# Kernel optimization log

Measured on AMD Instinct MI355X. Metric: run time of the kernel, lower is better.

Reference implementation:

```python
import jax, jax.numpy as jnp
import numpy as np

NT, NS, NF, NG, NH, ND, HS = 365, 128, 6, 16, 8, 366, 256
EPS = 1e-6


def _divide_p(p, t1, t2):
    # func.divideP: rain/snow partition via arccos temperature interpolation
    r = jnp.clip((t1 + t2) / jnp.maximum(t2 - t1, EPS), -1.0, 1.0)
    vf = jnp.arccos(r) / jnp.pi
    vf = jnp.where(t1 >= 0, 0.0, vf)
    vf = jnp.where(t2 <= 0, 1.0, vf)
    return p * vf, p * (1.0 - vf)  # Ps (snow), Pl (liquid)


def _hard_sigmoid(x):
    return jnp.clip(x / 6.0 + 0.5, 0.0, 1.0)


def setup_inputs():
    key = jax.random.key(0)
    ks = jax.random.split(key, 11)
    prcp = jax.random.uniform(ks[0], (NT, NS)) * 10.0
    evp = jax.random.uniform(ks[1], (NT, NS)) * 5.0
    t1 = jax.random.normal(ks[2], (NT, NS)) * 10.0
    t2 = t1 + jax.random.uniform(ks[3], (NT, NS)) * 10.0 + 0.1
    rad = jax.random.normal(ks[4], (NT, NS))
    hum = jax.random.normal(ks[5], (NT, NS))
    x = jnp.stack([prcp, evp, t1, t2, rad, hum], axis=-1)  # (NT, NS, 6)
    xc = jax.random.normal(ks[6], (NS, NG))

    def lin(k, fan_out, fan_in):
        b = 1.0 / np.sqrt(fan_in)
        kw, kb = jax.random.split(k)
        return (jax.random.uniform(kw, (fan_out, fan_in), minval=-b, maxval=b),
                jax.random.uniform(kb, (fan_out,), minval=-b, maxval=b))

    W_fc, b_fc = lin(ks[7], HS, NG)
    W_g, b_g = lin(ks[8], NH * 6, HS)
    W_kin, b_kin = lin(ks[9], HS, 4)
    W_kout, b_kout = lin(ks[10], NH * 1, HS)
    return dict(x=x, xc=xc, W_fc=W_fc, b_fc=b_fc, W_g=W_g, b_g=b_g,
                W_kin=W_kin, b_kin=b_kin, W_kout=W_kout, b_kout=b_kout)


def reference(x, xc, W_fc, b_fc, W_g, b_g, W_kin, b_kin, W_kout, b_kout):
    prcp, evp, t1, t2 = x[..., 0], x[..., 1], x[..., 2], x[..., 3]
    ps, pl = _divide_p(prcp, t1, t2)  # (NT, NS)
    f = x[..., 2:]  # (NT, NS, 4) time-varying features T1,T2,Rad,Hum

    # getParam (eval mode -> DropMask is identity)
    state = xc @ W_fc.T + b_fc                                   # (NS, HS)
    pk = jnp.tanh(f @ W_kin.T + b_kin + state) @ W_kout.T + b_kout  # (NT, NS, NH)
    pg = jnp.tanh(state) @ W_g.T + b_g                           # (NS, 6*NH)
    km = jnp.exp(pk)                                             # melt rate
    gk = jnp.exp(pg[:, 0:NH]) / 100.0                            # recession
    gl = jnp.exp(pg[:, NH:2 * NH]) * 100.0                       # capacity
    qb = jax.nn.relu(pg[:, 2 * NH:3 * NH]) / 10.0                # baseflow
    ga = jax.nn.softmax(pg[:, 3 * NH:4 * NH], axis=-1)           # bucket areas
    gi = _hard_sigmoid(pg[:, 4 * NH:5 * NH]) / 2.0               # infiltration frac
    ge = jax.nn.relu(pg[:, 5 * NH:6 * NH])                       # evap factor

    sf0 = jnp.zeros((NS, NH), x.dtype)
    d0 = jnp.zeros((NS, NH, ND), x.dtype)

    @jax.checkpoint
    def step(carry, inp):
        sf, d = carry
        ps_t, pl_t, ev_t, km_t = inp
        # snow bucket
        sf1 = sf + ps_t[:, None]
        melt = jnp.minimum(sf1, km_t)
        sf_new = sf1 - melt
        w_in = melt + pl_t[:, None] * gi           # inflow to soil (NS, NH)
        e_pot = ev_t[:, None] * ge
        # StorAge-Selection: age-rank shift, oldest bin pools
        d_sh = jnp.concatenate([w_in[..., None], d[..., :-1]], axis=-1)
        d_sh = d_sh.at[..., -1].add(d[..., -1])
        s = d_sh.sum(-1)
        # evaporation, uniform over ages, capped by storage
        f_ev = jnp.clip(e_pot / jnp.maximum(s, EPS), 0.0, 1.0)
        d1 = d_sh * (1.0 - f_ev[..., None])
        s1 = s * (1.0 - f_ev)
        # surface spill above capacity gl
        q_s = jax.nn.relu(s1 - gl)
        f_s = q_s / jnp.maximum(s1, EPS)
        d2 = d1 * (1.0 - f_s[..., None])
        s2 = s1 - q_s
        # uniform-SAS subsurface discharge
        q_sub = jnp.minimum(s2 * gk + qb, s2)
        f_q = q_sub / jnp.maximum(s2, EPS)
        q_age = d2 * f_q[..., None]                # flux[1]: per-age outflow
        q_age = q_age.at[..., 0].add(q_s)
        d_new = d2 * (1.0 - f_q[..., None])
        q = jnp.sum(q_age.sum(-1) * ga, axis=-1)   # area-weighted discharge (NS,)
        return (sf_new, d_new), q

    (_, _), q_pred = jax.lax.scan(step, (sf0, d0), (ps, pl, evp, km))
    return q_pred  # (NT, NS)
```

## Files before the change

kernel.cpp:

```cpp
#include <hip/hip_runtime.h>
#include <math.h>

#define NT 365
#define NT2 368
#define NS 128
#define NG 16
#define NH 8
#define HS 256
#define NSNH (NS * NH)
#define EPSC 1e-6f
#define TSTRIDE 96
#define TCH 46

#define WS_PRM 0
#define WS_P   8192

__device__ __forceinline__ float fast_rcp(float v) {
#if __has_builtin(__builtin_amdgcn_rcpf)
    return __builtin_amdgcn_rcpf(v);
#else
    return 1.f / v;
#endif
}
__device__ __forceinline__ float fast_tanh(float xv) {
    float e = __expf(2.f * xv);
    return 1.f - 2.f * fast_rcp(e + 1.f);
}
__device__ __forceinline__ float acos_over_pi(float r) {
    float ax = fabsf(r);
    float p = sqrtf(1.f - ax) *
              (0.49995890f + ax * (-0.06751697f + ax * (0.02363862f + ax * -0.00596153f)));
    return r < 0.f ? 1.f - p : p;
}

__global__ __launch_bounds__(256) void k_main(
    const float* __restrict__ x, const float* __restrict__ xc,
    const float* __restrict__ W_fc, const float* __restrict__ b_fc,
    const float* __restrict__ W_g, const float* __restrict__ b_g,
    const float* __restrict__ W_kin, const float* __restrict__ b_kin,
    const float* __restrict__ W_kout, const float* __restrict__ b_kout,
    float* __restrict__ prm, float* __restrict__ Pf)
{
    __shared__ float us[HS];
    __shared__ float ts[HS];
    __shared__ __align__(16) float4 wkin_lds[HS];
    __shared__ float wko_lds[8 * 260];
    __shared__ __align__(16) float lds_u[4 * 288];
    __shared__ float pgs[6 * NH];

    int tid = threadIdx.x;
    int wave = tid >> 6, lane = tid & 63;
    int s = blockIdx.x & 127;
    int t0 = (blockIdx.x >> 7) * 4 + wave;
    int h = lane >> 3, jg = lane & 7;

    wkin_lds[tid] = ((const float4*)W_kin)[tid];
#pragma unroll
    for (int i = 0; i < 8; ++i) {
        int idx = tid + 256 * i;
        wko_lds[(idx >> 8) * 260 + (idx & 255)] = W_kout[idx];
    }
    {
        float a = b_fc[tid];
        const float4* wf = (const float4*)(W_fc + tid * NG);
        const float* xr = xc + s * NG;
#pragma unroll
        for (int i = 0; i < 4; ++i) {
            float4 w = wf[i];
            a += xr[4*i] * w.x + xr[4*i+1] * w.y + xr[4*i+2] * w.z + xr[4*i+3] * w.w;
        }
        ts[tid] = fast_tanh(a);
        us[tid] = a + b_kin[tid];
    }
    __syncthreads();

    float ust[4]; float4 w4[4];
#pragma unroll
    for (int r = 0; r < 4; ++r) {
        ust[r] = us[lane + 64 * r];
        w4[r]  = wkin_lds[lane + 64 * r];
    }
    float4 wwr[8];
#pragma unroll
    for (int k = 0; k < 8; ++k)
        wwr[k] = *(const float4*)(wko_lds + h * 260 + jg * 32 + 4 * k);
    float bko = b_kout[h];

    if (blockIdx.x < NS) {
        for (int k = wave; k < 6 * NH; k += 4) {
            float p = 0.f;
#pragma unroll
            for (int r = 0; r < 4; ++r) {
                int jj = lane + 64 * r;
                p += ts[jj] * W_g[k * HS + jj];
            }
#pragma unroll
            for (int off = 32; off; off >>= 1) p += __shfl_xor(p, off, 64);
            if (lane == 0) pgs[k] = p + b_g[k];
        }
        __syncthreads();
        if (tid < NH) {
            int hh = tid;
            float gk = expf(pgs[hh]) * 0.01f;
            float gl = expf(pgs[NH + hh]) * 100.f;
            float qb = fmaxf(pgs[2 * NH + hh], 0.f) * 0.1f;
            float m = pgs[3 * NH];
#pragma unroll
            for (int i = 1; i < NH; ++i) m = fmaxf(m, pgs[3 * NH + i]);
            float den = 0.f;
#pragma unroll
            for (int i = 0; i < NH; ++i) den += expf(pgs[3 * NH + i] - m);
            float ga = expf(pgs[3 * NH + hh] - m) / den;
            float gi = fminf(fmaxf(pgs[4 * NH + hh] * (1.f / 6.f) + 0.5f, 0.f), 1.f) * 0.5f;
            float ge = fmaxf(pgs[5 * NH + hh], 0.f);
            int o = s * NH + hh;
            prm[0 * NSNH + o] = gk;
            prm[1 * NSNH + o] = gl;
            prm[2 * NSNH + o] = qb;
            prm[3 * NSNH + o] = ga;
            prm[4 * NSNH + o] = gi;
            prm[5 * NSNH + o] = ge;
        }
    }

    float* uw = lds_u + wave * 288;
    int ubase = lane + 4 * (lane >> 5);
    const float4* uuP = (const float4*)(uw + jg * 36);
    int sblk = s >> 3, srem = (s & 7) * 8;

#pragma unroll
    for (int g = 0; g < 8; ++g) {
        int t = t0 + 48 * g;
        float* Pt = Pf + (size_t)(sblk * NT2 + t) * TSTRIDE;
        if (t >= NT) {
            if (t < NT2) {
                if (jg == 0) Pt[srem + h] = 0.f;
                if (lane == 0)
                    ((float4*)(Pt + 64))[s & 7] = make_float4(0.f, 0.f, 0.f, 0.f);
            }
            continue;
        }
        const float2* xr2 = (const float2*)(x + (size_t)(t * NS + s) * 6);
        float2 a01 = xr2[0], a23 = xr2[1], a45 = xr2[2];
        float prcp = a01.x, ev = a01.y;
        float f0 = a23.x, f1 = a23.y, f2 = a45.x, f3 = a45.y;
#pragma unroll
        for (int r = 0; r < 4; ++r) {
            float uval = fast_tanh(ust[r] + f0 * w4[r].x + f1 * w4[r].y +
                                   f2 * w4[r].z + f3 * w4[r].w);
            uw[ubase + 72 * r] = uval;
        }
        float r_ = (f0 + f1) * fast_rcp(fmaxf(f1 - f0, EPSC));
        r_ = fminf(fmaxf(r_, -1.f), 1.f);
        float vf = acos_over_pi(r_);
        if (f0 >= 0.f) vf = 0.f;
        if (f1 <= 0.f) vf = 1.f;
        float psv = prcp * vf;
        float plv = prcp * (1.f - vf);
        float acc = 0.f;
#pragma unroll
        for (int k = 0; k < 8; ++k) {
            float4 a = uuP[k], b = wwr[k];
            acc += a.x * b.x + a.y * b.y + a.z * b.z + a.w * b.w;
        }
        acc += __shfl_xor(acc, 1, 64);
        acc += __shfl_xor(acc, 2, 64);
        acc += __shfl_xor(acc, 4, 64);
        if (jg == 0) Pt[srem + h] = __expf(acc + bko);
        if (lane == 0)
            ((float4*)(Pt + 64))[s & 7] = make_float4(psv, plv, ev, 0.f);
    }
}

__global__ __launch_bounds__(512, 1) void k_scan(
    const float* __restrict__ Pf, const float* __restrict__ prm,
    float* __restrict__ q)
{
    __shared__ float tup_sf[8][64][2];
    __shared__ __align__(16) float4 tup_S[8][64];
    __shared__ float region[8][64][17];

    int tid = threadIdx.x;
    int w = tid >> 6, lane = tid & 63;
    int blk = blockIdx.x;
    int sl = lane >> 3, ss0 = lane & 7;
    const float* Pb = Pf + (size_t)blk * (NT2 * TSTRIDE);
    int tbase = w * TCH;

    int gofs = blk * 64 + lane;
    float gk = prm[0 * NSNH + gofs];
    float gl = prm[1 * NSNH + gofs];
    float qb = prm[2 * NSNH + gofs];
    float gi = prm[4 * NSNH + gofs];
    float ge = prm[5 * NSNH + gofs];
    float c1 = 1.f - gk, nqb = -qb, nge = -ge;
    float hi = fmaxf(fmaf(gl, c1, nqb), 0.f);
    float gar[8];
#pragma unroll
    for (int hh = 0; hh < 8; ++hh)
        gar[hh] = prm[3 * NSNH + (blk * 8 + ss0) * 8 + hh];

    float u = 0.f, v = 0.f;
#define PHA(BASE, COUNT) _Pragma("unroll") \
    for (int c = 0; c < COUNT; ++c) { \
        const float* Pt = Pb + (tbase + BASE + c) * TSTRIDE; \
        float km = Pt[lane]; \
        float ps = Pt[64 + 4 * sl]; \
        float d = ps - km; \
        u = u + d; \
        v = fmaxf(v + d, 0.f); \
    }
    PHA(0, 16) PHA(16, 16) PHA(32, 14)
#undef PHA
    tup_sf[w][lane][0] = u; tup_sf[w][lane][1] = v;
    __syncthreads();

    float sfs = 0.f;
    for (int i = 0; i < w; ++i)
        sfs = fmaxf(sfs + tup_sf[i][lane][0], tup_sf[i][lane][1]);

    float aS = 1.f, bS = 0.f, lS = 0.f, hS = 1.0e30f;
    float sf = sfs;
#define PHB(BASE, COUNT) _Pragma("unroll") \
    for (int c = 0; c < COUNT; ++c) { \
        const float* Pt = Pb + (tbase + BASE + c) * TSTRIDE; \
        float km = Pt[lane]; \
        float4 a4 = ((const float4*)(Pt + 64))[sl]; \
        float sf1 = sf + a4.x; \
        float melt = fminf(sf1, km); \
        sf = sf1 - melt; \
        float b = fmaf(a4.z, nge, fmaf(a4.y, gi, melt)); \
        float beta = fmaf(b, c1, nqb); \
        aS = aS * c1; \
        bS = fmaf(bS, c1, beta); \
        lS = __builtin_amdgcn_fmed3f(fmaf(lS, c1, beta), 0.f, hi); \
        hS = __builtin_amdgcn_fmed3f(fmaf(hS, c1, beta), 0.f, hi); \
    }
    PHB(0, 16) PHB(16, 16) PHB(32, 14)
#undef PHB
    tup_S[w][lane] = make_float4(aS, bS, lS, hS);
    __syncthreads();

    float Ss = 0.f;
    for (int i = 0; i < w; ++i) {
        float4 tp = tup_S[i][lane];
        Ss = __builtin_amdgcn_fmed3f(fmaf(Ss, tp.x, tp.y), tp.z, tp.w);
    }

    float S = Ss;
    sf = sfs;
#define PHC(BASE, COUNT) { \
    _Pragma("unroll") for (int c = 0; c < 16; ++c) { \
        if (c < COUNT) { \
            const float* Pt = Pb + (tbase + BASE + c) * TSTRIDE; \
            float km = Pt[lane]; \
            float4 a4 = ((const float4*)(Pt + 64))[sl]; \
            float sf1 = sf + a4.x; \
            float melt = fminf(sf1, km); \
            sf = sf1 - melt; \
            float Sw = S + fmaf(a4.y, gi, melt); \
            float t2v = fmaf(a4.z, nge, Sw); \
            float S1 = fmaxf(t2v, 0.f); \
            float S2 = __builtin_amdgcn_fmed3f(t2v, 0.f, gl); \
            float Sn = fmaxf(fmaf(S2, c1, nqb), 0.f); \
            S = Sn; \
            region[w][lane][c] = S1 - Sn; \
        } \
    } \
    _Pragma("unroll") for (int it = 0; it < 2; ++it) { \
        int idx = it * 64 + lane; int cq = idx >> 3; \
        float sum = 0.f; \
        _Pragma("unroll") for (int hh = 0; hh < 8; ++hh) \
            sum = fmaf(gar[hh], region[w][ss0 * 8 + hh][cq], sum); \
        int t = tbase + BASE + cq; \
        if (cq < COUNT && t < NT) q[t * NS + blk * 8 + ss0] = sum; \
    } }
    PHC(0, 16) PHC(16, 16) PHC(32, 14)
#undef PHC
}

extern "C" void kernel_launch(void* const* d_in, const int* in_sizes, int n_in,
                              void* d_out, int out_size, void* d_ws, size_t ws_size,
                              hipStream_t stream)
{
    const float* x      = (const float*)d_in[0];
    const float* xc     = (const float*)d_in[1];
    const float* W_fc   = (const float*)d_in[2];
    const float* b_fc   = (const float*)d_in[3];
    const float* W_g    = (const float*)d_in[4];
    const float* b_g    = (const float*)d_in[5];
    const float* W_kin  = (const float*)d_in[6];
    const float* b_kin  = (const float*)d_in[7];
    const float* W_kout = (const float*)d_in[8];
    const float* b_kout = (const float*)d_in[9];
    float* q = (float*)d_out;

    float* ws  = (float*)d_ws;
    float* prm = ws + WS_PRM;
    float* Pf  = ws + WS_P;

    hipLaunchKernelGGL(k_main, dim3(1536), dim3(256), 0, stream,
                       x, xc, W_fc, b_fc, W_g, b_g, W_kin, b_kin,
                       W_kout, b_kout, prm, Pf);

    hipLaunchKernelGGL(k_scan, dim3(16), dim3(512), 0, stream,
                       Pf, prm, q);
}
```

Baseline: 32.44 us.

## Keep W_kout in registers and reduce per-lane partial products via LDS transpose

Each lane now holds its slice of W_kout in registers, so it computes partial dot products for all 8 heads directly from its own tanh outputs instead of writing u to LDS and re-reading it. Partials go through a double-buffered LDS tile for a transposed reduction, finished by three cross-lane shuffles. This drops the W_kout LDS staging and the u round trip but adds 32 weight registers per lane, plus strided global loads of W_kout at kernel start.

```diff
diff --git a/kernel.cpp b/kernel.cpp
--- a/kernel.cpp
+++ b/kernel.cpp
@@ -44,22 +44,16 @@
     __shared__ float us[HS];
     __shared__ float ts[HS];
     __shared__ __align__(16) float4 wkin_lds[HS];
-    __shared__ float wko_lds[8 * 260];
-    __shared__ __align__(16) float lds_u[4 * 288];
+    __shared__ __align__(16) float pl_lds[4][2][8][68];
     __shared__ float pgs[6 * NH];
 
     int tid = threadIdx.x;
     int wave = tid >> 6, lane = tid & 63;
     int s = blockIdx.x & 127;
     int t0 = (blockIdx.x >> 7) * 4 + wave;
-    int h = lane >> 3, jg = lane & 7;
+    int hq = lane & 7, gq = lane >> 3;
 
     wkin_lds[tid] = ((const float4*)W_kin)[tid];
-#pragma unroll
-    for (int i = 0; i < 8; ++i) {
-        int idx = tid + 256 * i;
-        wko_lds[(idx >> 8) * 260 + (idx & 255)] = W_kout[idx];
-    }
     {
         float a = b_fc[tid];
         const float4* wf = (const float4*)(W_fc + tid * NG);
@@ -80,11 +74,13 @@
         ust[r] = us[lane + 64 * r];
         w4[r]  = wkin_lds[lane + 64 * r];
     }
-    float4 wwr[8];
-#pragma unroll
-    for (int k = 0; k < 8; ++k)
-        wwr[k] = *(const float4*)(wko_lds + h * 260 + jg * 32 + 4 * k);
-    float bko = b_kout[h];
+    float w2[4][8];
+#pragma unroll
+    for (int r = 0; r < 4; ++r)
+#pragma unroll
+        for (int hh = 0; hh < 8; ++hh)
+            w2[r][hh] = W_kout[hh * HS + lane + 64 * r];
+    float bko = b_kout[hq];
 
     if (blockIdx.x < NS) {
         for (int k = wave; k < 6 * NH; k += 4) {
@@ -123,9 +119,6 @@
         }
     }
 
-    float* uw = lds_u + wave * 288;
-    int ubase = lane + 4 * (lane >> 5);
-    const float4* uuP = (const float4*)(uw + jg * 36);
     int sblk = s >> 3, srem = (s & 7) * 8;
 
 #pragma unroll
@@ -134,8 +127,8 @@
         float* Pt = Pf + (size_t)(sblk * NT2 + t) * TSTRIDE;
         if (t >= NT) {
             if (t < NT2) {
-                if (jg == 0) Pt[srem + h] = 0.f;
-                if (lane == 0)
+                if (lane < 8) Pt[srem + lane] = 0.f;
+                if (lane == 8)
                     ((float4*)(Pt + 64))[s & 7] = make_float4(0.f, 0.f, 0.f, 0.f);
             }
             continue;
@@ -144,12 +137,22 @@
         float2 a01 = xr2[0], a23 = xr2[1], a45 = xr2[2];
         float prcp = a01.x, ev = a01.y;
         float f0 = a23.x, f1 = a23.y, f2 = a45.x, f3 = a45.y;
+
+        float4 pa = make_float4(0.f, 0.f, 0.f, 0.f);
+        float4 pb = make_float4(0.f, 0.f, 0.f, 0.f);
 #pragma unroll
         for (int r = 0; r < 4; ++r) {
-            float uval = fast_tanh(ust[r] + f0 * w4[r].x + f1 * w4[r].y +
-                                   f2 * w4[r].z + f3 * w4[r].w);
-            uw[ubase + 72 * r] = uval;
-        }
+            float u = fast_tanh(ust[r] + f0 * w4[r].x + f1 * w4[r].y +
+                                f2 * w4[r].z + f3 * w4[r].w);
+            pa.x = fmaf(u, w2[r][0], pa.x); pa.y = fmaf(u, w2[r][1], pa.y);
+            pa.z = fmaf(u, w2[r][2], pa.z); pa.w = fmaf(u, w2[r][3], pa.w);
+            pb.x = fmaf(u, w2[r][4], pb.x); pb.y = fmaf(u, w2[r][5], pb.y);
+            pb.z = fmaf(u, w2[r][6], pb.z); pb.w = fmaf(u, w2[r][7], pb.w);
+        }
+        float* pw = &pl_lds[wave][g & 1][0][lane];
+        pw[0 * 68] = pa.x; pw[1 * 68] = pa.y; pw[2 * 68] = pa.z; pw[3 * 68] = pa.w;
+        pw[4 * 68] = pb.x; pw[5 * 68] = pb.y; pw[6 * 68] = pb.z; pw[7 * 68] = pb.w;
+
         float r_ = (f0 + f1) * fast_rcp(fmaxf(f1 - f0, EPSC));
         r_ = fminf(fmaxf(r_, -1.f), 1.f);
         float vf = acos_over_pi(r_);
@@ -157,17 +160,17 @@
         if (f1 <= 0.f) vf = 1.f;
         float psv = prcp * vf;
         float plv = prcp * (1.f - vf);
-        float acc = 0.f;
-#pragma unroll
-        for (int k = 0; k < 8; ++k) {
-            float4 a = uuP[k], b = wwr[k];
-            acc += a.x * b.x + a.y * b.y + a.z * b.z + a.w * b.w;
-        }
-        acc += __shfl_xor(acc, 1, 64);
-        acc += __shfl_xor(acc, 2, 64);
-        acc += __shfl_xor(acc, 4, 64);
-        if (jg == 0) Pt[srem + h] = __expf(acc + bko);
-        if (lane == 0)
+
+        const float4* pr = (const float4*)&pl_lds[wave][g & 1][hq][8 * gq];
+        float4 q0 = pr[0], q1 = pr[1];
+        float sumv = ((q0.x + q0.y) + (q0.z + q0.w)) +
+                     ((q1.x + q1.y) + (q1.z + q1.w));
+        sumv += __shfl_xor(sumv, 8, 64);
+        sumv += __shfl_xor(sumv, 16, 64);
+        sumv += __shfl_xor(sumv, 32, 64);
+
+        if (lane < 8) Pt[srem + lane] = __expf(sumv + bko);
+        if (lane == 8)
             ((float4*)(Pt + 64))[s & 7] = make_float4(psv, plv, ev, 0.f);
     }
 }
```

Result: no change. 32.68 us (+0.7%).
